# Optimization experiments

Hardware: AMD Instinct MI355X
Metric: run time of the kernel (lower is better)

## Reference

```python
import jax, jax.numpy as jnp
import numpy as np

B, S, D, H = 4, 2048, 1024, 16
DK = D // H  # 64


def setup_inputs() -> dict:
    key = jax.random.key(0)
    ks = jax.random.split(key, 5)
    scale = 1.0 / np.sqrt(D)
    return {
        "embeddings": jax.random.normal(ks[0], (B, S, D), dtype=jnp.float32),
        "W_q": jax.random.normal(ks[1], (D, D), dtype=jnp.float32) * scale,
        "W_k": jax.random.normal(ks[2], (D, D), dtype=jnp.float32) * scale,
        "W_v": jax.random.normal(ks[3], (D, D), dtype=jnp.float32) * scale,
        "W_o": jax.random.normal(ks[4], (D, D), dtype=jnp.float32) * scale,
    }


def reference(embeddings, W_q, W_k, W_v, W_o):
    # torch nn.Linear: y = x @ W.T  (weights are [out, in])
    b, s, d = embeddings.shape
    h, dk = H, DK
    q = embeddings @ W_q.T  # [b, s, d]
    k = embeddings @ W_k.T
    v = embeddings @ W_v.T
    # split heads along last dim (matches the per-head slicing in the torch loop)
    q = q.reshape(b, s, h, dk)
    k = k.reshape(b, s, h, dk)
    v = v.reshape(b, s, h, dk)
    scores = jnp.einsum("bqhd,bkhd->bhqk", q, k) / jnp.sqrt(jnp.float32(dk))
    p = jax.nn.softmax(scores, axis=-1)  # dropout is identity at eval
    ctx = jnp.einsum("bhqk,bkhd->bqhd", p, v).reshape(b, s, d)
    return ctx @ W_o.T
```

## Files before the change

### kernel.cpp

```cpp
#include <hip/hip_runtime.h>
#include <hip/hip_bf16.h>

typedef unsigned short u16;
typedef __attribute__((ext_vector_type(8))) short bf16x8;
typedef __attribute__((ext_vector_type(4))) float f32x4;

#define AS1 __attribute__((address_space(1)))
#define AS3 __attribute__((address_space(3)))

constexpr int Bc = 4, Sc = 2048, Dc = 1024, Hc = 16, DKc = 64;
constexpr size_t EDc = (size_t)Bc * Sc * Dc;
constexpr size_t WDc = (size_t)Dc * Dc;

__device__ __forceinline__ void g2l16(const void* g, void* l) {
  __builtin_amdgcn_global_load_lds((const AS1 unsigned int*)g,
                                   (AS3 unsigned int*)l, 16, 0, 0);
}

__device__ __forceinline__ u16 f2b(float f) {
  union { float f; unsigned u; } x; x.f = f;
  unsigned r = x.u + 0x7fffu + ((x.u >> 16) & 1u);
  return (u16)(r >> 16);
}

#if __has_builtin(__builtin_amdgcn_cvt_pk_bf16_f32)
typedef __attribute__((ext_vector_type(2))) __bf16 hbf2;
__device__ __forceinline__ unsigned f2b_pk(float a, float b) {
  union { hbf2 v; unsigned u; } x;
  x.v = __builtin_amdgcn_cvt_pk_bf16_f32(a, b);
  return x.u;
}
#else
__device__ __forceinline__ unsigned f2b_pk(float a, float b) {
  return (unsigned)f2b(a) | ((unsigned)f2b(b) << 16);
}
#endif

__device__ __forceinline__ float fast_exp2(float x) {
#if __has_builtin(__builtin_amdgcn_exp2f)
  return __builtin_amdgcn_exp2f(x);
#else
  return exp2f(x);
#endif
}

__global__ __launch_bounds__(256)
void cvt_all(const float* __restrict__ e, const float* __restrict__ wq,
             const float* __restrict__ wk, const float* __restrict__ wv,
             const float* __restrict__ wo, u16* __restrict__ dst) {
  int bx = blockIdx.x;
  const float* src;
  size_t doff;
  int chunk;
  if (bx < 4096) {
    src = e; doff = 0; chunk = bx;
  } else {
    int t = bx - 4096;
    int w = t >> 9;
    chunk = t & 511;
    src = (w == 0) ? wq : (w == 1) ? wk : (w == 2) ? wv : wo;
    doff = EDc + (size_t)w * WDc;
  }
  size_t i = ((size_t)chunk * 256 + threadIdx.x) * 8;
  float4 a = *(const float4*)(src + i);
  float4 b = *(const float4*)(src + i + 4);
  bf16x8 o;
  o[0] = (short)f2b(a.x); o[1] = (short)f2b(a.y);
  o[2] = (short)f2b(a.z); o[3] = (short)f2b(a.w);
  o[4] = (short)f2b(b.x); o[5] = (short)f2b(b.y);
  o[6] = (short)f2b(b.z); o[7] = (short)f2b(b.w);
  *(bf16x8*)(dst + doff + i) = o;
}

__global__ __launch_bounds__(256, 2)
void gemm_qkv(const u16* __restrict__ X, const u16* __restrict__ Wq,
              const u16* __restrict__ Wk, const u16* __restrict__ Wv,
              u16* __restrict__ Qo, u16* __restrict__ Ko,
              u16* __restrict__ VTo) {
  constexpr int BM = 128, BK = 64, K = Dc, N = Dc;
  __shared__ u16 As[BM * BK];
  __shared__ u16 Bs[BM * BK];

  const int tid = threadIdx.x;
  const int wave = tid >> 6, lane = tid & 63;
  const int mr = lane & 15, quad = lane >> 4, mr7 = lane & 7;
  const int sect = blockIdx.x >> 3;
  const int n0 = (blockIdx.x & 7) * 128;
  const int m0 = blockIdx.y * BM;
  const u16* W = (sect == 0) ? Wq : (sect == 1) ? Wk : Wv;
  const int wm = (wave >> 1) * 64, wn = (wave & 1) * 64;
  const int ldr = lane >> 3;
  const int ldc_sw = ((lane & 7) ^ (ldr & 7)) * 8;
  const bool vsec = (sect == 2);

  const f32x4 zero = {0.f, 0.f, 0.f, 0.f};
  f32x4 acc[4][4];
  #pragma unroll
  for (int i = 0; i < 4; i++)
    #pragma unroll
    for (int j = 0; j < 4; j++) acc[i][j] = zero;

  for (int k0 = 0; k0 < K; k0 += BK) {
    __syncthreads();
    #pragma unroll
    for (int i = 0; i < 4; i++) {
      int row = wave * 32 + i * 8;
      g2l16(X + (size_t)(m0 + row + ldr) * K + k0 + ldc_sw, As + row * BK);
      g2l16(W + (size_t)(n0 + row + ldr) * K + k0 + ldc_sw, Bs + row * BK);
    }
    __syncthreads();

    #pragma unroll
    for (int c = 0; c < 2; c++) {
      bf16x8 a[4], b[4];
      #pragma unroll
      for (int i = 0; i < 4; i++)
        a[i] = *(const bf16x8*)(As + (wm + i * 16 + mr) * BK +
                                (((c * 4 + quad) ^ mr7) * 8));
      #pragma unroll
      for (int j = 0; j < 4; j++)
        b[j] = *(const bf16x8*)(Bs + (wn + j * 16 + mr) * BK +
                                (((c * 4 + quad) ^ mr7) * 8));
      if (vsec) {
        #pragma unroll
        for (int i = 0; i < 4; i++)
          #pragma unroll
          for (int j = 0; j < 4; j++)
            acc[i][j] = __builtin_amdgcn_mfma_f32_16x16x32_bf16(
                b[j], a[i], acc[i][j], 0, 0, 0);
      } else {
        #pragma unroll
        for (int i = 0; i < 4; i++)
          #pragma unroll
          for (int j = 0; j < 4; j++)
            acc[i][j] = __builtin_amdgcn_mfma_f32_16x16x32_bf16(
                a[i], b[j], acc[i][j], 0, 0, 0);
      }
    }
  }

  if (vsec) {
    #pragma unroll
    for (int i = 0; i < 4; i++) {
      int s_glob = m0 + wm + i * 16 + mr;
      int bb = s_glob >> 11, s = s_glob & 2047;
      int sp = (s & ~63) | (s & 32) | ((s & 12) << 1) | ((s & 16) >> 2) |
               (s & 3);
      #pragma unroll
      for (int j = 0; j < 4; j++) {
        int nbase = n0 + wn + j * 16 + quad * 4;
        #pragma unroll
        for (int r = 0; r < 4; r++) {
          int n = nbase + r;
          int h = n >> 6, d = n & 63;
          VTo[((size_t)((bb * Hc + h) * DKc + d)) * Sc + sp] = f2b(acc[i][j][r]);
        }
      }
    }
  } else {
    const float scale = (sect == 0) ? 0.18033688f : 1.0f;
    u16* Y = (sect == 0) ? Qo : Ko;
    #pragma unroll
    for (int i = 0; i < 4; i++)
      #pragma unroll
      for (int j = 0; j < 4; j++)
        #pragma unroll
        for (int r = 0; r < 4; r++) {
          int m = m0 + wm + i * 16 + quad * 4 + r;
          int n = n0 + wn + j * 16 + mr;
          Y[(size_t)m * N + n] = f2b(acc[i][j][r] * scale);
        }
  }
}

__global__ __launch_bounds__(256, 2)
void gemm_out(const u16* __restrict__ X, const u16* __restrict__ W,
              float* __restrict__ Y, int M, int N, int K) {
  constexpr int BM = 128, BK = 64;
  __shared__ u16 As[BM * BK];
  __shared__ u16 Bs[BM * BK];

  const int tid = threadIdx.x;
  const int wave = tid >> 6, lane = tid & 63;
  const int mr = lane & 15, quad = lane >> 4, mr7 = lane & 7;
  const int m0 = blockIdx.y * BM, n0 = blockIdx.x * BM;
  const int wm = (wave >> 1) * 64, wn = (wave & 1) * 64;
  const int ldr = lane >> 3;
  const int ldc_sw = ((lane & 7) ^ (ldr & 7)) * 8;

  const f32x4 zero = {0.f, 0.f, 0.f, 0.f};
  f32x4 acc[4][4];
  #pragma unroll
  for (int i = 0; i < 4; i++)
    #pragma unroll
    for (int j = 0; j < 4; j++) acc[i][j] = zero;

  for (int k0 = 0; k0 < K; k0 += BK) {
    __syncthreads();
    #pragma unroll
    for (int i = 0; i < 4; i++) {
      int row = wave * 32 + i * 8;
      g2l16(X + (size_t)(m0 + row + ldr) * K + k0 + ldc_sw, As + row * BK);
      g2l16(W + (size_t)(n0 + row + ldr) * K + k0 + ldc_sw, Bs + row * BK);
    }
    __syncthreads();

    #pragma unroll
    for (int c = 0; c < 2; c++) {
      bf16x8 a[4], b[4];
      #pragma unroll
      for (int i = 0; i < 4; i++)
        a[i] = *(const bf16x8*)(As + (wm + i * 16 + mr) * BK +
                                (((c * 4 + quad) ^ mr7) * 8));
      #pragma unroll
      for (int j = 0; j < 4; j++)
        b[j] = *(const bf16x8*)(Bs + (wn + j * 16 + mr) * BK +
                                (((c * 4 + quad) ^ mr7) * 8));
      #pragma unroll
      for (int i = 0; i < 4; i++)
        #pragma unroll
        for (int j = 0; j < 4; j++)
          acc[i][j] = __builtin_amdgcn_mfma_f32_16x16x32_bf16(
              a[i], b[j], acc[i][j], 0, 0, 0);
    }
  }

  #pragma unroll
  for (int i = 0; i < 4; i++)
    #pragma unroll
    for (int j = 0; j < 4; j++)
      #pragma unroll
      for (int r = 0; r < 4; r++) {
        int m = m0 + wm + i * 16 + quad * 4 + r;
        int n = n0 + wn + j * 16 + mr;
        Y[(size_t)m * N + n] = acc[i][j][r];
      }
}

__global__ __launch_bounds__(512, 4)
void attn(const u16* __restrict__ Q, const u16* __restrict__ K,
          const u16* __restrict__ VT, u16* __restrict__ O) {
  __shared__ u16 Ks[2][64 * 64];
  __shared__ u16 Vs[2][64 * 64];

  const int tid = threadIdx.x;
  const int wave = tid >> 6, lane = tid & 63;
  const int mr = lane & 15, quad = lane >> 4, mr7 = lane & 7;
  const int bh = blockIdx.y;
  const int b = bh >> 4, h = bh & 15;
  const int q0 = blockIdx.x * 256;
  const size_t headK = (size_t)b * Sc * Dc + (size_t)h * DKc;
  const size_t headV = (size_t)bh * DKc * Sc;
  const int ldr = lane >> 3;
  const int ldc_sw = ((lane & 7) ^ (ldr & 7)) * 8;

  const int row0 = wave * 8;
  const int pr = row0 + ldr;

  bf16x8 qa[2][2];
  #pragma unroll
  for (int sub = 0; sub < 2; sub++)
    #pragma unroll
    for (int c = 0; c < 2; c++)
      qa[sub][c] = *(const bf16x8*)(Q + headK +
          (size_t)(q0 + wave * 32 + sub * 16 + mr) * Dc + c * 32 + quad * 8);

  const f32x4 zero = {0.f, 0.f, 0.f, 0.f};
  f32x4 o[2][4];
  float lsum[2];
  #pragma unroll
  for (int sub = 0; sub < 2; sub++) {
    lsum[sub] = 0.f;
    #pragma unroll
    for (int i = 0; i < 4; i++) o[sub][i] = zero;
  }

  g2l16(K + headK + (size_t)pr * Dc + ldc_sw, Ks[0] + row0 * 64);
  g2l16(VT + headV + (size_t)pr * Sc + ldc_sw, Vs[0] + row0 * 64);
  __syncthreads();

  union W8 { unsigned u[4]; bf16x8 v; };

  for (int kt = 0; kt < Sc / 64; kt++) {
    const int cur = kt & 1;
    if (kt + 1 < Sc / 64) {
      const int nk0 = (kt + 1) * 64;
      const int nxt = cur ^ 1;
      g2l16(K + headK + (size_t)(nk0 + pr) * Dc + ldc_sw, Ks[nxt] + row0 * 64);
      g2l16(VT + headV + (size_t)pr * Sc + nk0 + ldc_sw, Vs[nxt] + row0 * 64);
    }

    f32x4 s0[4], s1[4];
    #pragma unroll
    for (int kc = 0; kc < 4; kc++) {
      bf16x8 k0 = *(const bf16x8*)(Ks[cur] + (kc * 16 + mr) * 64 +
                                   ((quad ^ mr7) * 8));
      bf16x8 k1 = *(const bf16x8*)(Ks[cur] + (kc * 16 + mr) * 64 +
                                   (((4 + quad) ^ mr7) * 8));
      __builtin_amdgcn_s_setprio(1);
      s0[kc] = __builtin_amdgcn_mfma_f32_16x16x32_bf16(k0, qa[0][0], zero, 0, 0, 0);
      s1[kc] = __builtin_amdgcn_mfma_f32_16x16x32_bf16(k0, qa[1][0], zero, 0, 0, 0);
      s0[kc] = __builtin_amdgcn_mfma_f32_16x16x32_bf16(k1, qa[0][1], s0[kc], 0, 0, 0);
      s1[kc] = __builtin_amdgcn_mfma_f32_16x16x32_bf16(k1, qa[1][1], s1[kc], 0, 0, 0);
      __builtin_amdgcn_s_setprio(0);
    }

    W8 paw[2][2];
    {
      float e[16];
      #pragma unroll
      for (int kc = 0; kc < 4; kc++)
        #pragma unroll
        for (int r = 0; r < 4; r++)
          e[kc * 4 + r] = fast_exp2(s0[kc][r]);
      lsum[0] += ((e[0] + e[1]) + (e[2] + e[3])) +
                 ((e[4] + e[5]) + (e[6] + e[7])) +
                 ((e[8] + e[9]) + (e[10] + e[11])) +
                 ((e[12] + e[13]) + (e[14] + e[15]));
      paw[0][0].u[0] = f2b_pk(e[0], e[1]);
      paw[0][0].u[1] = f2b_pk(e[2], e[3]);
      paw[0][0].u[2] = f2b_pk(e[4], e[5]);
      paw[0][0].u[3] = f2b_pk(e[6], e[7]);
      paw[0][1].u[0] = f2b_pk(e[8], e[9]);
      paw[0][1].u[1] = f2b_pk(e[10], e[11]);
      paw[0][1].u[2] = f2b_pk(e[12], e[13]);
      paw[0][1].u[3] = f2b_pk(e[14], e[15]);
    }
    {
      float e[16];
      #pragma unroll
      for (int kc = 0; kc < 4; kc++)
        #pragma unroll
        for (int r = 0; r < 4; r++)
          e[kc * 4 + r] = fast_exp2(s1[kc][r]);
      lsum[1] += ((e[0] + e[1]) + (e[2] + e[3])) +
                 ((e[4] + e[5]) + (e[6] + e[7])) +
                 ((e[8] + e[9]) + (e[10] + e[11])) +
                 ((e[12] + e[13]) + (e[14] + e[15]));
      paw[1][0].u[0] = f2b_pk(e[0], e[1]);
      paw[1][0].u[1] = f2b_pk(e[2], e[3]);
      paw[1][0].u[2] = f2b_pk(e[4], e[5]);
      paw[1][0].u[3] = f2b_pk(e[6], e[7]);
      paw[1][1].u[0] = f2b_pk(e[8], e[9]);
      paw[1][1].u[1] = f2b_pk(e[10], e[11]);
      paw[1][1].u[2] = f2b_pk(e[12], e[13]);
      paw[1][1].u[3] = f2b_pk(e[14], e[15]);
    }

    #pragma unroll
    for (int ni = 0; ni < 4; ni++) {
      bf16x8 v0 = *(const bf16x8*)(Vs[cur] + (ni * 16 + mr) * 64 +
                                   ((quad ^ mr7) * 8));
      bf16x8 v1 = *(const bf16x8*)(Vs[cur] + (ni * 16 + mr) * 64 +
                                   (((4 + quad) ^ mr7) * 8));
      __builtin_amdgcn_s_setprio(1);
      o[0][ni] = __builtin_amdgcn_mfma_f32_16x16x32_bf16(
          paw[0][0].v, v0, o[0][ni], 0, 0, 0);
      o[1][ni] = __builtin_amdgcn_mfma_f32_16x16x32_bf16(
          paw[1][0].v, v0, o[1][ni], 0, 0, 0);
      o[0][ni] = __builtin_amdgcn_mfma_f32_16x16x32_bf16(
          paw[0][1].v, v1, o[0][ni], 0, 0, 0);
      o[1][ni] = __builtin_amdgcn_mfma_f32_16x16x32_bf16(
          paw[1][1].v, v1, o[1][ni], 0, 0, 0);
      __builtin_amdgcn_s_setprio(0);
    }

    __syncthreads();
  }

  #pragma unroll
  for (int sub = 0; sub < 2; sub++) {
    float l = lsum[sub];
    l += __shfl_xor(l, 16, 64);
    l += __shfl_xor(l, 32, 64);
    #pragma unroll
    for (int r = 0; r < 4; r++) {
      float inv = 1.0f / __shfl(l, quad * 4 + r, 64);
      int qq = q0 + wave * 32 + sub * 16 + quad * 4 + r;
      #pragma unroll
      for (int ni = 0; ni < 4; ni++)
        O[headK + (size_t)qq * Dc + ni * 16 + mr] = f2b(o[sub][ni][r] * inv);
    }
  }
}

extern "C" void kernel_launch(void* const* d_in, const int* in_sizes, int n_in,
                              void* d_out, int out_size, void* d_ws, size_t ws_size,
                              hipStream_t stream) {
  const float* emb = (const float*)d_in[0];
  const float* Wq  = (const float*)d_in[1];
  const float* Wk  = (const float*)d_in[2];
  const float* Wv  = (const float*)d_in[3];
  const float* Wo  = (const float*)d_in[4];
  float* out = (float*)d_out;

  const int M = Bc * Sc;

  u16* Eb  = (u16*)d_ws;
  u16* Wqb = Eb  + EDc;
  u16* Wkb = Wqb + WDc;
  u16* Wvb = Wkb + WDc;
  u16* Wob = Wvb + WDc;
  u16* Qb  = Wob + WDc;
  u16* Kb  = Qb  + EDc;
  u16* VTb = Kb  + EDc;
  u16* Cb  = Qb;

  dim3 blk(256);
  cvt_all<<<dim3(4096 + 4 * 512), blk, 0, stream>>>(emb, Wq, Wk, Wv, Wo, Eb);

  gemm_qkv<<<dim3(24, M / 128), blk, 0, stream>>>(Eb, Wqb, Wkb, Wvb,
                                                  Qb, Kb, VTb);

  attn<<<dim3(Sc / 256, Bc * Hc), dim3(512), 0, stream>>>(Qb, Kb, VTb, Cb);

  gemm_out<<<dim3(Dc / 128, M / 128), blk, 0, stream>>>(Cb, Wob, out,
                                                        M, Dc, Dc);
}
```

Baseline: 261.7 us.

## Compute softmax row sums via MFMA with ones and swizzle block order

The attention kernel no longer accumulates softmax denominators with scalar float adds and cross-lane shuffles. It now multiplies the bf16 probability fragments by a ones vector on MFMA, which yields row sums already in the output layout. All three kernels also remap the block index with an XCD-aware swizzle so neighbouring tiles share L2. The ones-MFMA trick adds four MFMAs per tile and sums the bf16-rounded probabilities rather than the fp32 ones, which slightly changes the normalisation.

```diff
diff --git a/kernel.cpp b/kernel.cpp
--- a/kernel.cpp
+++ b/kernel.cpp
@@ -84,9 +84,12 @@
   const int tid = threadIdx.x;
   const int wave = tid >> 6, lane = tid & 63;
   const int mr = lane & 15, quad = lane >> 4, mr7 = lane & 7;
-  const int sect = blockIdx.x >> 3;
-  const int n0 = (blockIdx.x & 7) * 128;
-  const int m0 = blockIdx.y * BM;
+  const int hwlin = blockIdx.y * 24 + blockIdx.x;
+  const int swz = (hwlin & 7) * 192 + (hwlin >> 3);
+  const int lx = swz % 24, ly = swz / 24;
+  const int sect = lx >> 3;
+  const int n0 = (lx & 7) * 128;
+  const int m0 = ly * BM;
   const u16* W = (sect == 0) ? Wq : (sect == 1) ? Wk : Wv;
   const int wm = (wave >> 1) * 64, wn = (wave & 1) * 64;
   const int ldr = lane >> 3;
@@ -183,7 +186,9 @@
   const int tid = threadIdx.x;
   const int wave = tid >> 6, lane = tid & 63;
   const int mr = lane & 15, quad = lane >> 4, mr7 = lane & 7;
-  const int m0 = blockIdx.y * BM, n0 = blockIdx.x * BM;
+  const int hwlin = blockIdx.y * 8 + blockIdx.x;
+  const int swz = (hwlin & 7) * 64 + (hwlin >> 3);
+  const int m0 = (swz >> 3) * BM, n0 = (swz & 7) * BM;
   const int wm = (wave >> 1) * 64, wn = (wave & 1) * 64;
   const int ldr = lane >> 3;
   const int ldc_sw = ((lane & 7) ^ (ldr & 7)) * 8;
@@ -246,9 +251,11 @@
   const int tid = threadIdx.x;
   const int wave = tid >> 6, lane = tid & 63;
   const int mr = lane & 15, quad = lane >> 4, mr7 = lane & 7;
-  const int bh = blockIdx.y;
+  const int hwlin = blockIdx.y * 8 + blockIdx.x;
+  const int swz = (hwlin & 7) * 64 + (hwlin >> 3);
+  const int bh = swz >> 3;
+  const int q0 = (swz & 7) * 256;
   const int b = bh >> 4, h = bh & 15;
-  const int q0 = blockIdx.x * 256;
   const size_t headK = (size_t)b * Sc * Dc + (size_t)h * DKc;
   const size_t headV = (size_t)bh * DKc * Sc;
   const int ldr = lane >> 3;
@@ -266,11 +273,14 @@
           (size_t)(q0 + wave * 32 + sub * 16 + mr) * Dc + c * 32 + quad * 8);
 
   const f32x4 zero = {0.f, 0.f, 0.f, 0.f};
+  const short one_bf = (short)0x3F80;
+  const bf16x8 ones = {one_bf, one_bf, one_bf, one_bf,
+                       one_bf, one_bf, one_bf, one_bf};
   f32x4 o[2][4];
-  float lsum[2];
+  f32x4 lacc[2];
   #pragma unroll
   for (int sub = 0; sub < 2; sub++) {
-    lsum[sub] = 0.f;
+    lacc[sub] = zero;
     #pragma unroll
     for (int i = 0; i < 4; i++) o[sub][i] = zero;
   }
@@ -313,10 +323,6 @@
         #pragma unroll
         for (int r = 0; r < 4; r++)
           e[kc * 4 + r] = fast_exp2(s0[kc][r]);
-      lsum[0] += ((e[0] + e[1]) + (e[2] + e[3])) +
-                 ((e[4] + e[5]) + (e[6] + e[7])) +
-                 ((e[8] + e[9]) + (e[10] + e[11])) +
-                 ((e[12] + e[13]) + (e[14] + e[15]));
       paw[0][0].u[0] = f2b_pk(e[0], e[1]);
       paw[0][0].u[1] = f2b_pk(e[2], e[3]);
       paw[0][0].u[2] = f2b_pk(e[4], e[5]);
@@ -333,10 +339,6 @@
         #pragma unroll
         for (int r = 0; r < 4; r++)
           e[kc * 4 + r] = fast_exp2(s1[kc][r]);
-      lsum[1] += ((e[0] + e[1]) + (e[2] + e[3])) +
-                 ((e[4] + e[5]) + (e[6] + e[7])) +
-                 ((e[8] + e[9]) + (e[10] + e[11])) +
-                 ((e[12] + e[13]) + (e[14] + e[15]));
       paw[1][0].u[0] = f2b_pk(e[0], e[1]);
       paw[1][0].u[1] = f2b_pk(e[2], e[3]);
       paw[1][0].u[2] = f2b_pk(e[4], e[5]);
@@ -346,6 +348,17 @@
       paw[1][1].u[2] = f2b_pk(e[12], e[13]);
       paw[1][1].u[3] = f2b_pk(e[14], e[15]);
     }
+
+    __builtin_amdgcn_s_setprio(1);
+    lacc[0] = __builtin_amdgcn_mfma_f32_16x16x32_bf16(
+        paw[0][0].v, ones, lacc[0], 0, 0, 0);
+    lacc[0] = __builtin_amdgcn_mfma_f32_16x16x32_bf16(
+        paw[0][1].v, ones, lacc[0], 0, 0, 0);
+    lacc[1] = __builtin_amdgcn_mfma_f32_16x16x32_bf16(
+        paw[1][0].v, ones, lacc[1], 0, 0, 0);
+    lacc[1] = __builtin_amdgcn_mfma_f32_16x16x32_bf16(
+        paw[1][1].v, ones, lacc[1], 0, 0, 0);
+    __builtin_amdgcn_s_setprio(0);
 
     #pragma unroll
     for (int ni = 0; ni < 4; ni++) {
@@ -370,12 +383,9 @@
 
   #pragma unroll
   for (int sub = 0; sub < 2; sub++) {
-    float l = lsum[sub];
-    l += __shfl_xor(l, 16, 64);
-    l += __shfl_xor(l, 32, 64);
     #pragma unroll
     for (int r = 0; r < 4; r++) {
-      float inv = 1.0f / __shfl(l, quad * 4 + r, 64);
+      float inv = 1.0f / lacc[sub][r];
       int qq = q0 + wave * 32 + sub * 16 + quad * 4 + r;
       #pragma unroll
       for (int ni = 0; ni < 4; ni++)
```

Measured after the change: 257.5 us. Within noise of the previous version (-1.6%).
